# Kernel optimization log

Measured on AMD Instinct MI355X. Metric: run time of the kernel, lower is better.

The kernel has to match this reference:

```python
import jax, jax.numpy as jnp
import numpy as np

B, U, T, H, D, K = 8, 512, 1024, 512, 128, 10

def setup_inputs() -> dict:
    key = jax.random.key(0)
    k1, k2, k3 = jax.random.split(key, 3)
    h_t = jax.random.normal(k1, (B, U, H), dtype=jnp.float32)
    ctx = jax.random.normal(k2, (B, T, D), dtype=jnp.float32)
    mask = jnp.ones((B, T), dtype=jnp.float32)
    # small init scale so exp(linear(h_t)) stays numerically tame
    W = jax.random.normal(k3, (H, 3 * K), dtype=jnp.float32) * 0.02
    b = jnp.zeros((3 * K,), dtype=jnp.float32)
    return {"h_t": h_t, "ctx": ctx, "mask": mask, "W": W, "b": b}

def reference(h_t, ctx, mask, W, b):
    # params = exp(Linear(h_t)) : [B, U, 3K]
    p = jnp.exp(h_t @ W + b)
    alpha, beta, kappa = jnp.split(p, 3, axis=-1)  # each [B, U, K]
    kappa = jnp.cumsum(kappa * 0.2, axis=1)        # monotone attention position
    u = jnp.arange(ctx.shape[1], dtype=jnp.float32)  # [T]
    # phi[b,u,t] = sum_k alpha * exp(-beta * (kappa - t)^2)
    diff = kappa[:, :, None, :] - u[None, None, :, None]          # [B, U, T, K]
    phi = jnp.sum(alpha[:, :, None, :] * jnp.exp(-beta[:, :, None, :] * diff * diff), axis=-1)  # [B, U, T]
    # masked weighted sum over ctx positions
    out = jnp.einsum('but,btd,bt->bud', phi, ctx, mask)           # [B, U, D]
    return out
```

## Files before the change

kernel.cpp:

```cpp
#include <hip/hip_runtime.h>
#include <math.h>

#define B_ 8
#define U_ 512
#define T_ 1024
#define H_ 512
#define D_ 128
#define K_ 10

#define UT 16
#define TC 32
#define NT2 32

typedef __attribute__((ext_vector_type(8))) short bf16x8;
typedef __attribute__((ext_vector_type(4))) float f32x4;

__device__ __forceinline__ unsigned short f32_to_bf16_rtne(float f) {
    unsigned u = __float_as_uint(f);
    unsigned r = u + 0x7FFFu + ((u >> 16) & 1u);
    return (unsigned short)(r >> 16);
}
__device__ __forceinline__ unsigned pack_bf16(float a, float b) {
    return (unsigned)f32_to_bf16_rtne(a) | ((unsigned)f32_to_bf16_rtne(b) << 16);
}

__device__ __forceinline__ unsigned long long pack_flag(float v) {
    unsigned lo = __float_as_uint(v);
    return ((unsigned long long)(lo ^ 0x80000000u) << 32) | lo;
}
__device__ __forceinline__ bool unpack_flag(unsigned long long g, float* v) {
    unsigned lo = (unsigned)g, hi = (unsigned)(g >> 32);
    *v = __uint_as_float(lo);
    return (hi == (lo ^ 0x80000000u)) && (*v > 0.f);
}

__global__ __launch_bounds__(512, 1)
void fused_kernel(const float* __restrict__ h_t,
                  const float* __restrict__ ctx,
                  const float* __restrict__ mask,
                  const float* __restrict__ W,
                  const float* __restrict__ bias,
                  float* __restrict__ out,
                  unsigned long long* __restrict__ Tg) {
    __shared__ unsigned short A_s[16 * 512];
    __shared__ float Cp[4][16][33];
    __shared__ float ab_s[16][20];
    __shared__ float kin_s[16][K_];
    __shared__ float L_s[16][K_];
    __shared__ float part_s[NT2][K_];
    __shared__ float pre_s[K_];
    __shared__ float phi_s[16][TC + 4];
    __shared__ float ctx_s[TC][D_];
    __shared__ float red_lo[160], red_hi[160];

    int tid = threadIdx.x;
    int lane = tid & 63;
    int w = tid >> 6;
    int b = blockIdx.x >> 5;
    int mytile = blockIdx.x & 31;
    int row0 = b * U_ + mytile * UT;

    int kq = w >> 1;
    int ntile = w & 1;
    int c = 16 * ntile + (lane & 15);
    int kb = kq * 128 + ((lane >> 4) << 3);
    bf16x8 bfrag[4];
    #pragma unroll
    for (int s = 0; s < 4; ++s) {
        #pragma unroll
        for (int e = 0; e < 8; ++e) {
            float wv = (c < 30) ? W[(size_t)(kb + 32 * s + e) * 30 + c] : 0.f;
            bfrag[s][e] = (short)f32_to_bf16_rtne(wv);
        }
    }

    {
        int r = tid >> 5;
        int kc = (tid & 31) * 16;
        const float4* src = (const float4*)(h_t + (size_t)(row0 + r) * H_ + kc);
        unsigned pk[8];
        #pragma unroll
        for (int i = 0; i < 4; ++i) {
            float4 v = src[i];
            pk[2 * i]     = pack_bf16(v.x, v.y);
            pk[2 * i + 1] = pack_bf16(v.z, v.w);
        }
        int base = r * 1024 + kc * 2;
        int swz = (r & 7) << 4;
        *(int4*)((char*)A_s + ((base) ^ swz)) =
            make_int4((int)pk[0], (int)pk[1], (int)pk[2], (int)pk[3]);
        *(int4*)((char*)A_s + ((base + 16) ^ swz)) =
            make_int4((int)pk[4], (int)pk[5], (int)pk[6], (int)pk[7]);
    }
    __syncthreads();

    {
        int ar = lane & 15;
        int abase = ar * 1024 + (kq * 128 + ((lane >> 4) << 3)) * 2;
        int aswz = (ar & 7) << 4;
        f32x4 acc = {0.f, 0.f, 0.f, 0.f};
        #pragma unroll
        for (int s = 0; s < 4; ++s) {
            bf16x8 af = *(const bf16x8*)((const char*)A_s + ((abase + s * 64) ^ aswz));
            acc = __builtin_amdgcn_mfma_f32_16x16x32_bf16(af, bfrag[s], acc, 0, 0, 0);
        }
        int rbase = (lane >> 4) * 4;
        int ccol = 16 * ntile + (lane & 15);
        #pragma unroll
        for (int r = 0; r < 4; ++r)
            Cp[kq][rbase + r][ccol] = acc[r];
    }
    __syncthreads();

    if (tid < 480) {
        int rr = tid / 30, cc = tid % 30;
        float dot = (Cp[0][rr][cc] + Cp[1][rr][cc]) + (Cp[2][rr][cc] + Cp[3][rr][cc]);
        float p = __expf(dot + bias[cc]);
        if (cc < 20) ab_s[rr][cc] = p;
        else         kin_s[rr][cc - 20] = 0.2f * p;
    }
    __syncthreads();

    if (tid < UT * K_) {
        int u_l = tid / K_, k = tid % K_;
        float ssum = 0.f;
        for (int r = 0; r <= u_l; ++r) ssum += kin_s[r][k];
        L_s[u_l][k] = ssum;
        if (u_l == UT - 1)
            __hip_atomic_store(&Tg[((size_t)b * NT2 + mytile) * K_ + k],
                               pack_flag(ssum),
                               __ATOMIC_RELAXED, __HIP_MEMORY_SCOPE_AGENT);
    }
    __syncthreads();

    if (tid < NT2 * K_) {
        int jg = tid / K_, k = tid % K_;
        float v = 0.f;
        if (jg < mytile) {
            const unsigned long long* p = &Tg[((size_t)b * NT2 + jg) * K_ + k];
            for (;;) {
                unsigned long long g = __hip_atomic_load(p, __ATOMIC_RELAXED,
                                                         __HIP_MEMORY_SCOPE_AGENT);
                if (unpack_flag(g, &v)) break;
                __builtin_amdgcn_s_sleep(1);
            }
        }
        part_s[jg][k] = v;
    }
    __syncthreads();
    if (tid < K_) {
        float pre = 0.f;
        #pragma unroll
        for (int jg = 0; jg < NT2; ++jg) pre += part_s[jg][tid];
        pre_s[tid] = pre;
    }
    __syncthreads();

    if (tid < UT * K_) {
        int u_l = tid / K_, k = tid % K_;
        float kv = pre_s[k] + L_s[u_l][k];
        kin_s[u_l][k] = kv;
        float bvv = ab_s[u_l][10 + k];
        float r = sqrtf(20.f / bvv);
        red_lo[tid] = kv - r; red_hi[tid] = kv + r;
    }
    __syncthreads();
    if (tid < 64) {
        float l = fminf(red_lo[tid], red_lo[tid + 64]);
        float h = fmaxf(red_hi[tid], red_hi[tid + 64]);
        if (tid < 32) { l = fminf(l, red_lo[tid + 128]); h = fmaxf(h, red_hi[tid + 128]); }
        #pragma unroll
        for (int d = 32; d > 0; d >>= 1) {
            l = fminf(l, __shfl_xor(l, d, 64));
            h = fmaxf(h, __shfl_xor(h, d, 64));
        }
        if (tid == 0) { red_lo[0] = l; red_hi[0] = h; }
    }
    __syncthreads();
    int t_begin = max(0, (int)floorf(red_lo[0]));
    int t_end   = min(T_, (int)ceilf(red_hi[0]) + 1);

    int u2 = tid >> 5;
    int g  = tid & 31;
    float a0[4] = {0.f, 0.f, 0.f, 0.f};
    float a1[4] = {0.f, 0.f, 0.f, 0.f};

    for (int t0 = t_begin; t0 < t_end; t0 += TC) {
        __syncthreads();
        {
            #pragma unroll
            for (int i = 0; i < (TC * D_ / 4) / 512; ++i) {
                int slot = tid + 512 * i;
                int r = slot >> 5;
                int rc = min(t0 + r, T_ - 1);
                const float4* src = (const float4*)(ctx + ((size_t)b * T_ + rc) * D_);
                ((float4*)(&ctx_s[0][0]))[slot] = src[slot & 31];
            }
        }
        {
            int uu = tid >> 5;
            int tl = tid & 31;
            int tf_i = t0 + tl;
            float tf = (float)tf_i;
            float ph = 0.f;
            #pragma unroll
            for (int k = 0; k < K_; ++k) {
                float d = kin_s[uu][k] - tf;
                float x = ab_s[uu][10 + k] * d * d;
                ph += ab_s[uu][k] * __expf(-x);
            }
            int tm = min(tf_i, T_ - 1);
            ph = (tf_i < T_) ? ph * mask[(size_t)b * T_ + tm] : 0.f;
            phi_s[uu][tl] = ph;
        }
        __syncthreads();
        if (tid < 256) {
            for (int tl4 = 0; tl4 < TC / 4; ++tl4) {
                float4 p0 = *(const float4*)(&phi_s[u2][4 * tl4]);
                float4 p1 = *(const float4*)(&phi_s[u2 + 8][4 * tl4]);
                #pragma unroll
                for (int qq = 0; qq < 4; ++qq) {
                    float f0 = (qq == 0) ? p0.x : (qq == 1) ? p0.y : (qq == 2) ? p0.z : p0.w;
                    float f1 = (qq == 0) ? p1.x : (qq == 1) ? p1.y : (qq == 2) ? p1.z : p1.w;
                    float4 c0 = ((const float4*)(&ctx_s[4 * tl4 + qq][0]))[g];
                    a0[0] += f0 * c0.x; a0[1] += f0 * c0.y;
                    a0[2] += f0 * c0.z; a0[3] += f0 * c0.w;
                    a1[0] += f1 * c0.x; a1[1] += f1 * c0.y;
                    a1[2] += f1 * c0.z; a1[3] += f1 * c0.w;
                }
            }
        }
    }

    if (tid < 256) {
        float* orow0 = out + ((size_t)(b * U_ + mytile * UT) + u2) * D_;
        float* orow1 = out + ((size_t)(b * U_ + mytile * UT) + u2 + 8) * D_;
        *(float4*)(orow0 + 4 * g) = make_float4(a0[0], a0[1], a0[2], a0[3]);
        *(float4*)(orow1 + 4 * g) = make_float4(a1[0], a1[1], a1[2], a1[3]);
    }
}

extern "C" void kernel_launch(void* const* d_in, const int* in_sizes, int n_in,
                              void* d_out, int out_size, void* d_ws, size_t ws_size,
                              hipStream_t stream) {
    const float* h_t  = (const float*)d_in[0];
    const float* ctx  = (const float*)d_in[1];
    const float* mask = (const float*)d_in[2];
    const float* W    = (const float*)d_in[3];
    const float* bias = (const float*)d_in[4];
    float* out = (float*)d_out;
    unsigned long long* Tg = (unsigned long long*)d_ws;

    fused_kernel<<<dim3(B_ * NT2), dim3(512), 0, stream>>>(
        h_t, ctx, mask, W, bias, out, Tg);
}
```

Baseline: 13.04 us.

## Double-buffer ctx/phi chunks with warp-specialized producer and consumer halves

Splits the 512 threads so the first 256 accumulate the current chunk while the other 256 load the next ctx chunk and compute its phi values into a second shared buffer. This halves the barriers per chunk and overlaps global loads and exp work with the FMA accumulation. In exchange the producer half does twice the per-thread work, and shared memory grows for the doubled buffers.

```diff
diff --git a/kernel.cpp b/kernel.cpp
--- a/kernel.cpp
+++ b/kernel.cpp
@@ -49,8 +49,8 @@
     __shared__ float L_s[16][K_];
     __shared__ float part_s[NT2][K_];
     __shared__ float pre_s[K_];
-    __shared__ float phi_s[16][TC + 4];
-    __shared__ float ctx_s[TC][D_];
+    __shared__ float phi_s[2][16][TC + 4];
+    __shared__ float ctx_s[2][TC][D_];
     __shared__ float red_lo[160], red_hi[160];
 
     int tid = threadIdx.x;
@@ -179,23 +179,22 @@
     __syncthreads();
     int t_begin = max(0, (int)floorf(red_lo[0]));
     int t_end   = min(T_, (int)ceilf(red_hi[0]) + 1);
+    int nch = (t_begin < t_end) ? ((t_end - t_begin + TC - 1) / TC) : 0;
 
     int u2 = tid >> 5;
     int g  = tid & 31;
     float a0[4] = {0.f, 0.f, 0.f, 0.f};
     float a1[4] = {0.f, 0.f, 0.f, 0.f};
 
-    for (int t0 = t_begin; t0 < t_end; t0 += TC) {
-        __syncthreads();
-        {
-            #pragma unroll
-            for (int i = 0; i < (TC * D_ / 4) / 512; ++i) {
-                int slot = tid + 512 * i;
-                int r = slot >> 5;
-                int rc = min(t0 + r, T_ - 1);
-                const float4* src = (const float4*)(ctx + ((size_t)b * T_ + rc) * D_);
-                ((float4*)(&ctx_s[0][0]))[slot] = src[slot & 31];
-            }
+    if (nch > 0) {
+        int t0 = t_begin;
+        #pragma unroll
+        for (int i = 0; i < 2; ++i) {
+            int slot = tid + 512 * i;
+            int r = slot >> 5;
+            int rc = min(t0 + r, T_ - 1);
+            const float4* src = (const float4*)(ctx + ((size_t)b * T_ + rc) * D_);
+            ((float4*)(&ctx_s[0][0][0]))[slot] = src[slot & 31];
         }
         {
             int uu = tid >> 5;
@@ -206,30 +205,63 @@
             #pragma unroll
             for (int k = 0; k < K_; ++k) {
                 float d = kin_s[uu][k] - tf;
-                float x = ab_s[uu][10 + k] * d * d;
-                ph += ab_s[uu][k] * __expf(-x);
+                ph += ab_s[uu][k] * __expf(-(ab_s[uu][10 + k] * d * d));
             }
             int tm = min(tf_i, T_ - 1);
             ph = (tf_i < T_) ? ph * mask[(size_t)b * T_ + tm] : 0.f;
-            phi_s[uu][tl] = ph;
-        }
-        __syncthreads();
+            phi_s[0][uu][tl] = ph;
+        }
+    }
+    __syncthreads();
+
+    for (int ci = 0; ci < nch; ++ci) {
+        int cur = ci & 1;
         if (tid < 256) {
             for (int tl4 = 0; tl4 < TC / 4; ++tl4) {
-                float4 p0 = *(const float4*)(&phi_s[u2][4 * tl4]);
-                float4 p1 = *(const float4*)(&phi_s[u2 + 8][4 * tl4]);
+                float4 p0 = *(const float4*)(&phi_s[cur][u2][4 * tl4]);
+                float4 p1 = *(const float4*)(&phi_s[cur][u2 + 8][4 * tl4]);
                 #pragma unroll
                 for (int qq = 0; qq < 4; ++qq) {
                     float f0 = (qq == 0) ? p0.x : (qq == 1) ? p0.y : (qq == 2) ? p0.z : p0.w;
                     float f1 = (qq == 0) ? p1.x : (qq == 1) ? p1.y : (qq == 2) ? p1.z : p1.w;
-                    float4 c0 = ((const float4*)(&ctx_s[4 * tl4 + qq][0]))[g];
+                    float4 c0 = ((const float4*)(&ctx_s[cur][4 * tl4 + qq][0]))[g];
                     a0[0] += f0 * c0.x; a0[1] += f0 * c0.y;
                     a0[2] += f0 * c0.z; a0[3] += f0 * c0.w;
                     a1[0] += f1 * c0.x; a1[1] += f1 * c0.y;
                     a1[2] += f1 * c0.z; a1[3] += f1 * c0.w;
                 }
             }
-        }
+        } else if (ci + 1 < nch) {
+            int t0 = t_begin + (ci + 1) * TC;
+            int nxt = cur ^ 1;
+            int t2 = tid - 256;
+            #pragma unroll
+            for (int i = 0; i < 4; ++i) {
+                int slot = t2 + 256 * i;
+                int r = slot >> 5;
+                int rc = min(t0 + r, T_ - 1);
+                const float4* src = (const float4*)(ctx + ((size_t)b * T_ + rc) * D_);
+                ((float4*)(&ctx_s[nxt][0][0]))[slot] = src[slot & 31];
+            }
+            #pragma unroll
+            for (int i = 0; i < 2; ++i) {
+                int o = t2 + 256 * i;
+                int uu = o >> 5;
+                int tl = o & 31;
+                int tf_i = t0 + tl;
+                float tf = (float)tf_i;
+                float ph = 0.f;
+                #pragma unroll
+                for (int k = 0; k < K_; ++k) {
+                    float d = kin_s[uu][k] - tf;
+                    ph += ab_s[uu][k] * __expf(-(ab_s[uu][10 + k] * d * d));
+                }
+                int tm = min(tf_i, T_ - 1);
+                ph = (tf_i < T_) ? ph * mask[(size_t)b * T_ + tm] : 0.f;
+                phi_s[nxt][uu][tl] = ph;
+            }
+        }
+        __syncthreads();
     }
 
     if (tid < 256) {
```

After: 13.12 us. Within noise of the previous version (+0.6%).
